# Kernel optimization log

Measured on AMD Instinct MI355X. Metric: run time of the kernel, lower is better.

Reference implementation:

```python
import jax, jax.numpy as jnp
import numpy as np

DEPTH = 6
IN_DIM = 768
NODE_HIDDEN = 16
LEAF_HIDDEN = 128
OUT_DIM = 768
BATCH = 4096
N_NODES = 2 ** DEPTH - 1   # 63 gating MLPs (heap/BFS order, root first)
N_LEAVES = 2 ** DEPTH      # 64 leaf MLPs


def setup_inputs() -> dict:
    key = jax.random.key(0)
    ks = jax.random.split(key, 5)
    def winit(k, shape, fan_in):
        return jax.random.normal(k, shape, jnp.float32) * (1.0 / np.sqrt(fan_in))
    return {
        "x": jax.random.normal(ks[0], (BATCH, IN_DIM), jnp.float32),
        "node_w1": winit(ks[1], (N_NODES, IN_DIM, NODE_HIDDEN), IN_DIM),
        "node_b1": jnp.zeros((N_NODES, NODE_HIDDEN), jnp.float32),
        "node_w2": winit(ks[2], (N_NODES, NODE_HIDDEN, 1), NODE_HIDDEN),
        "node_b2": jnp.zeros((N_NODES, 1), jnp.float32),
        "leaf_w1": winit(ks[3], (N_LEAVES, IN_DIM, LEAF_HIDDEN), IN_DIM),
        "leaf_b1": jnp.zeros((N_LEAVES, LEAF_HIDDEN), jnp.float32),
        "leaf_w2": winit(ks[4], (N_LEAVES, LEAF_HIDDEN, OUT_DIM), LEAF_HIDDEN),
        "leaf_b2": jnp.zeros((N_LEAVES, OUT_DIM), jnp.float32),
    }


def reference(x, node_w1, node_b1, node_w2, node_b2,
              leaf_w1, leaf_b1, leaf_w2, leaf_b2):
    """Training-mode (soft-gating) FFF tree, fully batched over all nodes/leaves.

    Equivalent to the recursive torch forward with training=True and the
    stochastic output-swap disabled (swap is a training-noise trick).
    """
    B = x.shape[0]
    # All node gates in one pass: c[b, n] = sigmoid(W2 @ relu(W1 @ x + b1) + b2)
    hn = jax.nn.relu(jnp.einsum('bi,nih->bnh', x, node_w1) + node_b1)
    c = jax.nn.sigmoid(jnp.einsum('bnh,nho->bno', hn, node_w2) + node_b2)[..., 0]  # [B, N_NODES]
    # All leaf MLPs in one pass (identity out activation)
    hl = jax.nn.relu(jnp.einsum('bi,lih->blh', x, leaf_w1) + leaf_b1)             # [B, L, LEAF_HIDDEN]
    y = jnp.einsum('blh,lho->blo', hl, leaf_w2) + leaf_b2                         # [B, L, OUT]
    # Leaf mixture weights: product of c (left) / (1-c) (right) along root->leaf path.
    # Heap index idx has children 2*idx, 2*idx+1; gate c weights the LEFT child.
    w = jnp.ones((B, 1), x.dtype)
    for lvl in range(DEPTH):
        g = c[:, 2 ** lvl - 1: 2 ** (lvl + 1) - 1]        # gates at this level, [B, 2^lvl]
        w = jnp.stack([w * g, w * (1.0 - g)], axis=-1).reshape(B, 2 ** (lvl + 1))
    return jnp.einsum('bl,blo->bo', w, y)                 # [B, OUT]
```

## Files before the change

kernel.cpp:

```cpp
#include <hip/hip_runtime.h>
#include <stdint.h>
#include <stddef.h>

typedef __attribute__((ext_vector_type(8))) short short8;
typedef __attribute__((ext_vector_type(4))) float f32x4;
typedef __attribute__((ext_vector_type(4))) short short4v;

__device__ __forceinline__ short f2bf(float f) {
  unsigned u = __builtin_bit_cast(unsigned, f);
  u = (u + 0x7fffu + ((u >> 16) & 1u)) >> 16;
  return (short)u;
}

__device__ __forceinline__ float bf2f(short s) {
  unsigned u = ((unsigned)(unsigned short)s) << 16;
  return __builtin_bit_cast(float, u);
}

__device__ __forceinline__ void gload16(const void* g, void* l) {
  __builtin_amdgcn_global_load_lds(
      (const __attribute__((address_space(1))) unsigned int*)g,
      (__attribute__((address_space(3))) unsigned int*)l, 16, 0, 0);
}


__global__ __launch_bounds__(256)
void cvt_misc_k(const float* __restrict__ x, const float* __restrict__ nw1,
                const float* __restrict__ lb2, short* __restrict__ xb,
                short* __restrict__ BTn, short* __restrict__ BT2) {
  const int bx = blockIdx.x;
  if (bx < 3072) {
    const int i = bx * 256 + threadIdx.x;
    const float4 v = ((const float4*)x)[i];
    short4v o;
    o.x = f2bf(v.x); o.y = f2bf(v.y); o.z = f2bf(v.z); o.w = f2bf(v.w);
    *(short4v*)(xb + (size_t)i * 4) = o;
  } else if (bx < 6144) {
    const int idx = (bx - 3072) * 256 + threadIdx.x;
    const int i = idx % 768;
    const int nh = idx / 768;
    float v = 0.f;
    if (nh < 1008) v = nw1[((size_t)(nh >> 4) * 768 + i) * 16 + (nh & 15)];
    BTn[idx] = f2bf(v);
  } else {
    const int idx = (bx - 6144) * 256 + threadIdx.x;
    const int o = idx >> 6, l = idx & 63;
    BT2[(size_t)o * 8256 + 8192 + l] = f2bf(lb2[(size_t)l * 768 + o]);
  }
}

__global__ __launch_bounds__(256, 4)
void node_cvt_k(const short* __restrict__ xb, const short* __restrict__ BTn,
                float* __restrict__ hn, const float* __restrict__ lw1,
                const float* __restrict__ lw2, short* __restrict__ BT1,
                short* __restrict__ BT2) {
  __shared__ char sh[24576];
  const int tid = threadIdx.x;
  if (blockIdx.x < 512) {
    constexpr int ABYTES = 64 * 128;
    const int lane = tid & 63, wid = tid >> 6;
    const int wm = wid >> 1, wn = wid & 1;
    const int sid = (blockIdx.x & 7) * 64 + (blockIdx.x >> 3);
    const int xg = sid % 8, yg = sid / 8;
    const int m0 = yg * 64, n0 = xg * 128;
    f32x4 acc[2][4];
    const f32x4 zero = {0.f, 0.f, 0.f, 0.f};
#pragma unroll
    for (int i = 0; i < 2; ++i)
#pragma unroll
      for (int j = 0; j < 4; ++j) acc[i][j] = zero;
    for (int ki = 0; ki < 12; ++ki) {
      const int k0 = ki * 64;
      __syncthreads();
#pragma unroll
      for (int s = 0; s < 6; ++s) {
        const int off = s * 4096 + tid * 16;
        const short* src;
        if (off < ABYTES) {
          const int r = off >> 7;
          const int cs = ((off >> 4) & 7) ^ (r & 7);
          src = xb + (size_t)(m0 + r) * 768 + k0 + cs * 8;
        } else {
          const int o2 = off - ABYTES;
          const int r = o2 >> 7;
          const int cs = ((o2 >> 4) & 7) ^ (r & 7);
          src = BTn + (size_t)(n0 + r) * 768 + k0 + cs * 8;
        }
        gload16(src, sh + off);
      }
      __syncthreads();
#pragma unroll
      for (int kk = 0; kk < 2; ++kk) {
        const int chunk = kk * 4 + (lane >> 4);
        short8 af[2], bfr[4];
#pragma unroll
        for (int i = 0; i < 2; ++i) {
          const int row = wm * 32 + i * 16 + (lane & 15);
          af[i] = *(const short8*)(sh + row * 128 + ((chunk ^ (row & 7)) << 4));
        }
#pragma unroll
        for (int j = 0; j < 4; ++j) {
          const int row = wn * 64 + j * 16 + (lane & 15);
          bfr[j] = *(const short8*)(sh + ABYTES + row * 128 + ((chunk ^ (row & 7)) << 4));
        }
#pragma unroll
        for (int i = 0; i < 2; ++i)
#pragma unroll
          for (int j = 0; j < 4; ++j)
            acc[i][j] = __builtin_amdgcn_mfma_f32_16x16x32_bf16(af[i], bfr[j], acc[i][j], 0, 0, 0);
      }
    }
    const int row_base = m0 + wm * 32 + (lane >> 4) * 4;
    const int col_base = n0 + wn * 64 + (lane & 15);
#pragma unroll
    for (int i = 0; i < 2; ++i)
#pragma unroll
      for (int j = 0; j < 4; ++j)
#pragma unroll
        for (int r = 0; r < 4; ++r)
          hn[(size_t)(row_base + i * 16 + r) * 1024 + col_base + j * 16] = acc[i][j][r];
  } else {
    float (*tile)[65] = (float(*)[65])sh;
    const int cb = blockIdx.x - 512;
    const int z = cb / 24, rem = cb % 24;
    const int by = rem / 12, bxx = rem % 12;
    const int h0 = by * 64, i0 = bxx * 64;
    if (z < 64) {
      const int l = z;
#pragma unroll
      for (int t = 0; t < 16; ++t) {
        const int e = t * 256 + tid;
        const int ii = e >> 6, hh = e & 63;
        tile[ii][hh] = lw1[(size_t)l * 98304 + (size_t)(i0 + ii) * 128 + (h0 + hh)];
      }
      __syncthreads();
#pragma unroll
      for (int t = 0; t < 16; ++t) {
        const int e = t * 256 + tid;
        const int hh = e >> 6, ii = e & 63;
        BT1[(size_t)(l * 128 + h0 + hh) * 768 + i0 + ii] = f2bf(tile[ii][hh]);
      }
    } else {
      const int l = z - 64;
      const int o0 = i0;
#pragma unroll
      for (int t = 0; t < 16; ++t) {
        const int e = t * 256 + tid;
        const int hh = e >> 6, oo = e & 63;
        tile[hh][oo] = lw2[(size_t)l * 98304 + (size_t)(h0 + hh) * 768 + (o0 + oo)];
      }
      __syncthreads();
#pragma unroll
      for (int t = 0; t < 16; ++t) {
        const int e = t * 256 + tid;
        const int oo = e >> 6, hh = e & 63;
        BT2[(size_t)(o0 + oo) * 8256 + l * 128 + h0 + hh] = f2bf(tile[hh][oo]);
      }
    }
  }
}

__global__ __launch_bounds__(256)
void gates_k(const float* __restrict__ hn, const float* __restrict__ nb1,
             const float* __restrict__ nw2, const float* __restrict__ nb2,
             float* __restrict__ wgt, short* __restrict__ hs) {
  const int b = blockIdx.x * 4 + (threadIdx.x >> 6);
  const int lane = threadIdx.x & 63;
  float c = 0.f;
  if (lane < 63) {
    float s = nb2[lane];
    const float* h = hn + (size_t)b * 1024 + lane * 16;
#pragma unroll
    for (int j = 0; j < 16; ++j) {
      float v = fmaxf(h[j] + nb1[lane * 16 + j], 0.f);
      s += v * nw2[lane * 16 + j];
    }
    c = 1.f / (1.f + expf(-s));
  }
  float w = 1.f;
#pragma unroll
  for (int lvl = 0; lvl < 6; ++lvl) {
    const int idx = (1 << lvl) - 1 + (lane >> (6 - lvl));
    const float g = __shfl(c, idx, 64);
    w *= ((lane >> (5 - lvl)) & 1) ? (1.f - g) : g;
  }
  wgt[(size_t)b * 64 + lane] = w;
  hs[(size_t)b * 8256 + 8192 + lane] = f2bf(w);
}

template <int EPI>
__global__ __launch_bounds__(512, 2)
void gemm8x(const short* __restrict__ A, const short* __restrict__ B,
            void* __restrict__ C0, float* __restrict__ P1, float* __restrict__ P2,
            short* __restrict__ Q1, short* __restrict__ Q2,
            const float* __restrict__ bias, const float* __restrict__ wgt) {
  constexpr int LDA = EPI ? 768 : 8256;
  constexpr int LDB = EPI ? 768 : 8256;
  constexpr int LDC = EPI ? 8256 : 768;
  constexpr int ABYTES = 256 * 128;
  constexpr int TILEB = 2 * ABYTES;
  __shared__ char lds[2 * TILEB];

  const int tid = threadIdx.x, lane = tid & 63, wid = tid >> 6;
  const int wm = wid >> 2, wn = wid & 3;

  const int c = blockIdx.x & 7, ii = blockIdx.x >> 3;
  int xg, yg, kt0, GKT, zz;
  if constexpr (EPI == 1) {
    xg = ((c & 3) << 3) + (ii & 7);
    yg = ((c >> 2) << 3) + (ii >> 3);
    kt0 = 0; GKT = 12; zz = 0;
  } else {
    const int uid = c * 30 + ii;
    zz = uid / 48;
    const int r = uid % 48;
    xg = r % 3; yg = r / 3;
    kt0 = zz * 26;
    GKT = (zz == 4) ? 25 : 26;
  }
  const int m0 = yg * 256, n0 = xg * 256;

  f32x4 acc[8][4];
  const f32x4 zero = {0.f, 0.f, 0.f, 0.f};
#pragma unroll
  for (int i = 0; i < 8; ++i)
#pragma unroll
    for (int j = 0; j < 4; ++j) acc[i][j] = zero;

  auto STG = [&](int buf, int mat, int h, int gk) {
    const int k0 = (kt0 + gk) * 64;
    char* dst = lds + buf * TILEB + mat * ABYTES + h * 16384;
    const short* base = mat ? B : A;
    const int ld = mat ? LDB : LDA;
    const int r0 = (mat ? n0 : m0) + h * 128;
#pragma unroll
    for (int s = 0; s < 2; ++s) {
      const int off = s * 8192 + tid * 16;
      const int r = off >> 7;
      const int cs = ((off >> 4) & 7) ^ (r & 7);
      gload16(base + (size_t)(r0 + r) * ld + k0 + cs * 8, dst + off);
    }
  };

  short8 bfrag[4][2];
  auto RD_B = [&](int buf) {
    const char* bB = lds + buf * TILEB + ABYTES;
#pragma unroll
    for (int j = 0; j < 4; ++j)
#pragma unroll
      for (int kk = 0; kk < 2; ++kk) {
        const int row = wn * 64 + j * 16 + (lane & 15);
        const int chunk = kk * 4 + (lane >> 4);
        bfrag[j][kk] = *(const short8*)(bB + row * 128 + ((chunk ^ (row & 7)) << 4));
      }
  };

  auto PH = [&](int buf, int q, bool rdB, int vm, auto&& stages) {
    if (rdB) RD_B(buf);
    const char* bA = lds + buf * TILEB;
    short8 af[2][2];
#pragma unroll
    for (int i = 0; i < 2; ++i)
#pragma unroll
      for (int kk = 0; kk < 2; ++kk) {
        const int row = wm * 128 + q * 32 + i * 16 + (lane & 15);
        const int chunk = kk * 4 + (lane >> 4);
        af[i][kk] = *(const short8*)(bA + row * 128 + ((chunk ^ (row & 7)) << 4));
      }
    stages();
    if (vm == 4) asm volatile("s_waitcnt vmcnt(4)" ::: "memory");
    else if (vm == 0) asm volatile("s_waitcnt vmcnt(0)" ::: "memory");
    __builtin_amdgcn_s_barrier();
    __builtin_amdgcn_s_setprio(1);
#pragma unroll
    for (int kk = 0; kk < 2; ++kk)
#pragma unroll
      for (int i = 0; i < 2; ++i)
#pragma unroll
        for (int j = 0; j < 4; ++j)
          acc[q * 2 + i][j] =
              __builtin_amdgcn_mfma_f32_16x16x32_bf16(af[i][kk], bfrag[j][kk], acc[q * 2 + i][j], 0, 0, 0);
    __builtin_amdgcn_s_setprio(0);
    __builtin_amdgcn_s_barrier();
  };

  STG(0, 0, 0, 0); STG(0, 0, 1, 0); STG(0, 1, 0, 0); STG(0, 1, 1, 0);
  STG(1, 1, 0, 1); STG(1, 1, 1, 1);
  asm volatile("s_waitcnt vmcnt(4)" ::: "memory");
  __builtin_amdgcn_s_barrier();

  const int iters = GKT >> 1;
  for (int it = 0; it < iters; ++it) {
    const int t0 = it * 2;
    const bool s2 = t0 + 2 < GKT, s3 = t0 + 3 < GKT;
    PH(0, 0, true, -1, [&] { STG(1, 0, 0, t0 + 1); });
    PH(0, 1, false, -1, [&] {
      STG(1, 0, 1, t0 + 1);
      if (s2) STG(0, 1, 0, t0 + 2);
    });
    PH(0, 2, false, -1, [&] { if (s2) STG(0, 1, 1, t0 + 2); });
    PH(0, 3, false, s2 ? 4 : 0, [] {});
    PH(1, 0, true, -1, [&] { if (s2) STG(0, 0, 0, t0 + 2); });
    PH(1, 1, false, -1, [&] { if (s2) STG(0, 0, 1, t0 + 2); });
    PH(1, 2, false, -1, [&] { if (s3) STG(1, 1, 0, t0 + 3); });
    PH(1, 3, false, s2 ? 4 : -1, [&] { if (s3) STG(1, 1, 1, t0 + 3); });
  }
  if (GKT & 1) {
    asm volatile("s_waitcnt vmcnt(0)" ::: "memory");
    __builtin_amdgcn_s_barrier();
    RD_B(0);
    const char* bA = lds;
#pragma unroll
    for (int q = 0; q < 4; ++q) {
      short8 af[2][2];
#pragma unroll
      for (int i = 0; i < 2; ++i)
#pragma unroll
        for (int kk = 0; kk < 2; ++kk) {
          const int row = wm * 128 + q * 32 + i * 16 + (lane & 15);
          const int chunk = kk * 4 + (lane >> 4);
          af[i][kk] = *(const short8*)(bA + row * 128 + ((chunk ^ (row & 7)) << 4));
        }
      __builtin_amdgcn_s_setprio(1);
#pragma unroll
      for (int kk = 0; kk < 2; ++kk)
#pragma unroll
        for (int i = 0; i < 2; ++i)
#pragma unroll
          for (int j = 0; j < 4; ++j)
            acc[q * 2 + i][j] =
                __builtin_amdgcn_mfma_f32_16x16x32_bf16(af[i][kk], bfrag[j][kk], acc[q * 2 + i][j], 0, 0, 0);
      __builtin_amdgcn_s_setprio(0);
    }
  }

  if constexpr (EPI == 1) {
    short* C = (short*)C0;
#pragma unroll
    for (int mi = 0; mi < 8; ++mi) {
      const int row_base = m0 + wm * 128 + mi * 16 + (lane >> 4) * 4;
#pragma unroll
      for (int j = 0; j < 4; ++j) {
        const int col = n0 + wn * 64 + j * 16 + (lane & 15);
        const int leaf = col >> 7;
        const float b = bias[col];
#pragma unroll
        for (int r = 0; r < 4; ++r) {
          const int row = row_base + r;
          const float v = fmaxf(acc[mi][j][r] + b, 0.f) * wgt[(size_t)row * 64 + leaf];
          C[(size_t)row * LDC + col] = f2bf(v);
        }
      }
    }
  } else {
    if (zz <= 2) {
      float* C = (zz == 0) ? (float*)C0 : (zz == 1 ? P1 : P2);
#pragma unroll
      for (int mi = 0; mi < 8; ++mi) {
        const int row_base = m0 + wm * 128 + mi * 16 + (lane >> 4) * 4;
#pragma unroll
        for (int j = 0; j < 4; ++j) {
          const int col = n0 + wn * 64 + j * 16 + (lane & 15);
#pragma unroll
          for (int r = 0; r < 4; ++r)
            C[(size_t)(row_base + r) * LDC + col] = acc[mi][j][r];
        }
      }
    } else {
      short* Q = (zz == 3) ? Q1 : Q2;
#pragma unroll
      for (int mi = 0; mi < 8; ++mi) {
        const int row_base = m0 + wm * 128 + mi * 16 + (lane >> 4) * 4;
#pragma unroll
        for (int j = 0; j < 4; ++j) {
          const int col = n0 + wn * 64 + j * 16 + (lane & 15);
#pragma unroll
          for (int r = 0; r < 4; ++r)
            Q[(size_t)(row_base + r) * LDC + col] = f2bf(acc[mi][j][r]);
        }
      }
    }
  }
}

__global__ __launch_bounds__(256)
void reduce_k(float* __restrict__ out, const float* __restrict__ p1,
              const float* __restrict__ p2, const short* __restrict__ q1,
              const short* __restrict__ q2) {
  const int i = blockIdx.x * 256 + threadIdx.x;
  f32x4 a = ((const f32x4*)out)[i];
  f32x4 b = ((const f32x4*)p1)[i];
  f32x4 c = ((const f32x4*)p2)[i];
  const short4v s1 = ((const short4v*)q1)[i];
  const short4v s2 = ((const short4v*)q2)[i];
  f32x4 r;
  r.x = (a.x + b.x) + (c.x + bf2f(s1.x) + bf2f(s2.x));
  r.y = (a.y + b.y) + (c.y + bf2f(s1.y) + bf2f(s2.y));
  r.z = (a.z + b.z) + (c.z + bf2f(s1.z) + bf2f(s2.z));
  r.w = (a.w + b.w) + (c.w + bf2f(s1.w) + bf2f(s2.w));
  ((f32x4*)out)[i] = r;
}


extern "C" void kernel_launch(void* const* d_in, const int* in_sizes, int n_in,
                              void* d_out, int out_size, void* d_ws, size_t ws_size,
                              hipStream_t stream) {
  const float* x   = (const float*)d_in[0];
  const float* nw1 = (const float*)d_in[1];
  const float* nb1 = (const float*)d_in[2];
  const float* nw2 = (const float*)d_in[3];
  const float* nb2 = (const float*)d_in[4];
  const float* lw1 = (const float*)d_in[5];
  const float* lb1 = (const float*)d_in[6];
  const float* lw2 = (const float*)d_in[7];
  const float* lb2 = (const float*)d_in[8];

  char* ws = (char*)d_ws;
  short* xb  = (short*)(ws + 0);
  short* BT1 = (short*)(ws + 6291456);
  short* BTn = (short*)(ws + 18874368);
  float* hn  = (float*)(ws + 20447232);
  float* wgt = (float*)(ws + 37224448);
  short* BT2 = (short*)(ws + 38273024);
  short* hs  = (short*)(ws + 50954240);
  float* p1  = (float*)(ws + 0);
  float* p2  = (float*)(ws + 12582912);
  short* q1  = (short*)(ws + 25165824);
  short* q2  = (short*)(ws + 31457280);

  cvt_misc_k<<<6336, 256, 0, stream>>>(x, nw1, lb2, xb, BTn, BT2);
  node_cvt_k<<<3584, 256, 0, stream>>>(xb, BTn, hn, lw1, lw2, BT1, BT2);

  gates_k<<<1024, 256, 0, stream>>>(hn, nb1, nw2, nb2, wgt, hs);

  gemm8x<1><<<512, 512, 0, stream>>>(xb, BT1, hs, nullptr, nullptr, nullptr,
                                     nullptr, lb1, wgt);

  gemm8x<0><<<240, 512, 0, stream>>>(hs, BT2, d_out, p1, p2, q1, q2,
                                     nullptr, nullptr);

  reduce_k<<<3072, 256, 0, stream>>>((float*)d_out, p1, p2, q1, q2);
}
```

Before: 155.6 us.

## Double GEMM block to 16 waves with 64x64 per-wave tiles

Both GEMM kernels now run with 1024 threads per block instead of 512. Each wave computes a 64x64 sub-tile instead of 128x64, which halves the accumulator registers per wave. Global-to-LDS staging is spread over twice as many threads, so each thread issues one 16-byte load per stage instead of two, and the vmcnt waits drop from 4 to 2 to match. The aim is more resident waves per CU to hide memory and LDS latency. The cost is that every wave still loads the full B fragment set for half as much MFMA work, so LDS read traffic per FLOP rises and barrier synchronisation now spans more waves.

```diff
diff --git a/kernel.cpp b/kernel.cpp
--- a/kernel.cpp
+++ b/kernel.cpp
@@ -189,8 +189,8 @@
 }
 
 template <int EPI>
-__global__ __launch_bounds__(512, 2)
-void gemm8x(const short* __restrict__ A, const short* __restrict__ B,
+__global__ __launch_bounds__(1024)
+void gemm8y(const short* __restrict__ A, const short* __restrict__ B,
             void* __restrict__ C0, float* __restrict__ P1, float* __restrict__ P2,
             short* __restrict__ Q1, short* __restrict__ Q2,
             const float* __restrict__ bias, const float* __restrict__ wgt) {
@@ -220,10 +220,10 @@
   }
   const int m0 = yg * 256, n0 = xg * 256;
 
-  f32x4 acc[8][4];
+  f32x4 acc[4][4];
   const f32x4 zero = {0.f, 0.f, 0.f, 0.f};
 #pragma unroll
-  for (int i = 0; i < 8; ++i)
+  for (int i = 0; i < 4; ++i)
 #pragma unroll
     for (int j = 0; j < 4; ++j) acc[i][j] = zero;
 
@@ -233,13 +233,10 @@
     const short* base = mat ? B : A;
     const int ld = mat ? LDB : LDA;
     const int r0 = (mat ? n0 : m0) + h * 128;
-#pragma unroll
-    for (int s = 0; s < 2; ++s) {
-      const int off = s * 8192 + tid * 16;
-      const int r = off >> 7;
-      const int cs = ((off >> 4) & 7) ^ (r & 7);
-      gload16(base + (size_t)(r0 + r) * ld + k0 + cs * 8, dst + off);
-    }
+    const int off = tid * 16;
+    const int r = off >> 7;
+    const int cs = ((off >> 4) & 7) ^ (r & 7);
+    gload16(base + (size_t)(r0 + r) * ld + k0 + cs * 8, dst + off);
   };
 
   short8 bfrag[4][2];
@@ -258,35 +255,30 @@
   auto PH = [&](int buf, int q, bool rdB, int vm, auto&& stages) {
     if (rdB) RD_B(buf);
     const char* bA = lds + buf * TILEB;
-    short8 af[2][2];
-#pragma unroll
-    for (int i = 0; i < 2; ++i)
-#pragma unroll
-      for (int kk = 0; kk < 2; ++kk) {
-        const int row = wm * 128 + q * 32 + i * 16 + (lane & 15);
-        const int chunk = kk * 4 + (lane >> 4);
-        af[i][kk] = *(const short8*)(bA + row * 128 + ((chunk ^ (row & 7)) << 4));
-      }
+    short8 af[2];
+#pragma unroll
+    for (int kk = 0; kk < 2; ++kk) {
+      const int row = wm * 64 + q * 16 + (lane & 15);
+      const int chunk = kk * 4 + (lane >> 4);
+      af[kk] = *(const short8*)(bA + row * 128 + ((chunk ^ (row & 7)) << 4));
+    }
     stages();
-    if (vm == 4) asm volatile("s_waitcnt vmcnt(4)" ::: "memory");
+    if (vm == 2) asm volatile("s_waitcnt vmcnt(2)" ::: "memory");
     else if (vm == 0) asm volatile("s_waitcnt vmcnt(0)" ::: "memory");
     __builtin_amdgcn_s_barrier();
     __builtin_amdgcn_s_setprio(1);
 #pragma unroll
     for (int kk = 0; kk < 2; ++kk)
 #pragma unroll
-      for (int i = 0; i < 2; ++i)
-#pragma unroll
-        for (int j = 0; j < 4; ++j)
-          acc[q * 2 + i][j] =
-              __builtin_amdgcn_mfma_f32_16x16x32_bf16(af[i][kk], bfrag[j][kk], acc[q * 2 + i][j], 0, 0, 0);
+      for (int j = 0; j < 4; ++j)
+        acc[q][j] = __builtin_amdgcn_mfma_f32_16x16x32_bf16(af[kk], bfrag[j][kk], acc[q][j], 0, 0, 0);
     __builtin_amdgcn_s_setprio(0);
     __builtin_amdgcn_s_barrier();
   };
 
   STG(0, 0, 0, 0); STG(0, 0, 1, 0); STG(0, 1, 0, 0); STG(0, 1, 1, 0);
   STG(1, 1, 0, 1); STG(1, 1, 1, 1);
-  asm volatile("s_waitcnt vmcnt(4)" ::: "memory");
+  asm volatile("s_waitcnt vmcnt(2)" ::: "memory");
   __builtin_amdgcn_s_barrier();
 
   const int iters = GKT >> 1;
@@ -299,11 +291,11 @@
       if (s2) STG(0, 1, 0, t0 + 2);
     });
     PH(0, 2, false, -1, [&] { if (s2) STG(0, 1, 1, t0 + 2); });
-    PH(0, 3, false, s2 ? 4 : 0, [] {});
+    PH(0, 3, false, s2 ? 2 : 0, [] {});
     PH(1, 0, true, -1, [&] { if (s2) STG(0, 0, 0, t0 + 2); });
     PH(1, 1, false, -1, [&] { if (s2) STG(0, 0, 1, t0 + 2); });
     PH(1, 2, false, -1, [&] { if (s3) STG(1, 1, 0, t0 + 3); });
-    PH(1, 3, false, s2 ? 4 : -1, [&] { if (s3) STG(1, 1, 1, t0 + 3); });
+    PH(1, 3, false, s2 ? 2 : -1, [&] { if (s3) STG(1, 1, 1, t0 + 3); });
   }
   if (GKT & 1) {
     asm volatile("s_waitcnt vmcnt(0)" ::: "memory");
@@ -312,24 +304,19 @@
     const char* bA = lds;
 #pragma unroll
     for (int q = 0; q < 4; ++q) {
-      short8 af[2][2];
-#pragma unroll
-      for (int i = 0; i < 2; ++i)
-#pragma unroll
-        for (int kk = 0; kk < 2; ++kk) {
-          const int row = wm * 128 + q * 32 + i * 16 + (lane & 15);
-          const int chunk = kk * 4 + (lane >> 4);
-          af[i][kk] = *(const short8*)(bA + row * 128 + ((chunk ^ (row & 7)) << 4));
-        }
+      short8 af[2];
+#pragma unroll
+      for (int kk = 0; kk < 2; ++kk) {
+        const int row = wm * 64 + q * 16 + (lane & 15);
+        const int chunk = kk * 4 + (lane >> 4);
+        af[kk] = *(const short8*)(bA + row * 128 + ((chunk ^ (row & 7)) << 4));
+      }
       __builtin_amdgcn_s_setprio(1);
 #pragma unroll
       for (int kk = 0; kk < 2; ++kk)
 #pragma unroll
-        for (int i = 0; i < 2; ++i)
-#pragma unroll
-          for (int j = 0; j < 4; ++j)
-            acc[q * 2 + i][j] =
-                __builtin_amdgcn_mfma_f32_16x16x32_bf16(af[i][kk], bfrag[j][kk], acc[q * 2 + i][j], 0, 0, 0);
+        for (int j = 0; j < 4; ++j)
+          acc[q][j] = __builtin_amdgcn_mfma_f32_16x16x32_bf16(af[kk], bfrag[j][kk], acc[q][j], 0, 0, 0);
       __builtin_amdgcn_s_setprio(0);
     }
   }
@@ -337,8 +324,8 @@
   if constexpr (EPI == 1) {
     short* C = (short*)C0;
 #pragma unroll
-    for (int mi = 0; mi < 8; ++mi) {
-      const int row_base = m0 + wm * 128 + mi * 16 + (lane >> 4) * 4;
+    for (int mi = 0; mi < 4; ++mi) {
+      const int row_base = m0 + wm * 64 + mi * 16 + (lane >> 4) * 4;
 #pragma unroll
       for (int j = 0; j < 4; ++j) {
         const int col = n0 + wn * 64 + j * 16 + (lane & 15);
@@ -356,8 +343,8 @@
     if (zz <= 2) {
       float* C = (zz == 0) ? (float*)C0 : (zz == 1 ? P1 : P2);
 #pragma unroll
-      for (int mi = 0; mi < 8; ++mi) {
-        const int row_base = m0 + wm * 128 + mi * 16 + (lane >> 4) * 4;
+      for (int mi = 0; mi < 4; ++mi) {
+        const int row_base = m0 + wm * 64 + mi * 16 + (lane >> 4) * 4;
 #pragma unroll
         for (int j = 0; j < 4; ++j) {
           const int col = n0 + wn * 64 + j * 16 + (lane & 15);
@@ -369,8 +356,8 @@
     } else {
       short* Q = (zz == 3) ? Q1 : Q2;
 #pragma unroll
-      for (int mi = 0; mi < 8; ++mi) {
-        const int row_base = m0 + wm * 128 + mi * 16 + (lane >> 4) * 4;
+      for (int mi = 0; mi < 4; ++mi) {
+        const int row_base = m0 + wm * 64 + mi * 16 + (lane >> 4) * 4;
 #pragma unroll
         for (int j = 0; j < 4; ++j) {
           const int col = n0 + wn * 64 + j * 16 + (lane & 15);
@@ -433,11 +420,11 @@
 
   gates_k<<<1024, 256, 0, stream>>>(hn, nb1, nw2, nb2, wgt, hs);
 
-  gemm8x<1><<<512, 512, 0, stream>>>(xb, BT1, hs, nullptr, nullptr, nullptr,
-                                     nullptr, lb1, wgt);
-
-  gemm8x<0><<<240, 512, 0, stream>>>(hs, BT2, d_out, p1, p2, q1, q2,
-                                     nullptr, nullptr);
+  gemm8y<1><<<512, 1024, 0, stream>>>(xb, BT1, hs, nullptr, nullptr, nullptr,
+                                      nullptr, lb1, wgt);
+
+  gemm8y<0><<<240, 1024, 0, stream>>>(hs, BT2, d_out, p1, p2, q1, q2,
+                                      nullptr, nullptr);
 
   reduce_k<<<3072, 256, 0, stream>>>((float*)d_out, p1, p2, q1, q2);
 }
```

Measured after the change: 199.7 us. 28.3% more time.
